# Kernel tuning notes

Hardware: AMD Instinct MI355X
Metric: run time of the kernel (lower is better)

Reference implementation:

```python
import jax, jax.numpy as jnp
import numpy as np

B, T_MEL, F_BINS, C = 32, 1024, 4, 256
S_PHONES = 256
MAX_DUR = 8


def setup_inputs() -> dict:
    key = jax.random.key(0)
    k1, k2 = jax.random.split(key)
    e_src = jax.random.normal(k1, (B, T_MEL, F_BINS, C), dtype=jnp.float32)
    d_src = jax.random.randint(k2, (B, S_PHONES), 0, MAX_DUR, dtype=jnp.int64)
    return {"e_src": e_src, "d_src": d_src}


def reference(e_src, d_src):
    # e_src: [B, T, F, C] prosody features; d_src: [B, S] phone durations (frames).
    # Original: agg[b, i] = mean over dims (0,1) of e_src[b, start_i:start_i+d_i],
    # i.e. mean over (frames_of_phone_i, freq); zeros if the slice is empty.
    Bd, T, Fb, Cd = e_src.shape
    S = d_src.shape[1]
    x = e_src.mean(axis=2)  # [B, T, C] mean over freq (uniform, commutes with frame mean)
    cum = jnp.cumsum(d_src, axis=1)  # [B, S] phone boundary ends
    t = jnp.arange(T)
    # frame -> phone id; frames beyond total duration go to dump segment S
    sid = jax.vmap(lambda c: jnp.searchsorted(c, t, side="right"))(cum)  # [B, T]

    def per_utt(xi, si):
        ssum = jax.ops.segment_sum(xi, si, num_segments=S + 1)[:S]  # [S, C]
        cnt = jax.ops.segment_sum(jnp.ones((T,), xi.dtype), si, num_segments=S + 1)[:S]
        return ssum, cnt

    seg_sum, counts = jax.vmap(per_utt)(x, sid)  # [B,S,C], [B,S]
    mean = seg_sum / jnp.maximum(counts, 1.0)[..., None]
    return jnp.where(counts[..., None] > 0, mean, jnp.zeros((), x.dtype))
```

## Files before the change

### kernel.cpp

```cpp
#include <hip/hip_runtime.h>


#define NB 32
#define NT 1024
#define NF 4
#define NC 256
#define NS 256

__global__ __launch_bounds__(256) void FastSpeech2Pros_83769042141888_kernel(
    const float* __restrict__ e_src,
    const int*   __restrict__ d_src,
    float*       __restrict__ out)
{
    const int s = blockIdx.x;
    const int b = blockIdx.y;
    const int t = threadIdx.x;

    __shared__ int cs[NS];
    cs[t] = d_src[b * NS + t];
    __syncthreads();
    #pragma unroll
    for (int off = 1; off < NS; off <<= 1) {
        int v = (t >= off) ? cs[t - off] : 0;
        __syncthreads();
        cs[t] += v;
        __syncthreads();
    }

    int end   = cs[s];
    int start = (s == 0) ? 0 : cs[s - 1];
    if (start > NT) start = NT;
    if (end   > NT) end   = NT;
    const int cnt = end - start;

    float4 acc = make_float4(0.f, 0.f, 0.f, 0.f);
    const float4* base =
        (const float4*)(e_src + (size_t)b * NT * NF * NC);
    for (int fr = start; fr < end; ++fr) {
        float4 v = base[(size_t)fr * (NF * NC / 4) + t];
        acc.x += v.x; acc.y += v.y; acc.z += v.z; acc.w += v.w;
    }

    __shared__ float4 red[256];
    red[t] = acc;
    __syncthreads();

    if (t < 64) {
        float4 a0 = red[t];
        float4 a1 = red[t + 64];
        float4 a2 = red[t + 128];
        float4 a3 = red[t + 192];
        const float inv = (cnt > 0) ? (1.0f / (4.0f * (float)cnt)) : 0.0f;
        float4 o;
        o.x = (a0.x + a1.x + a2.x + a3.x) * inv;
        o.y = (a0.y + a1.y + a2.y + a3.y) * inv;
        o.z = (a0.z + a1.z + a2.z + a3.z) * inv;
        o.w = (a0.w + a1.w + a2.w + a3.w) * inv;
        ((float4*)(out + ((size_t)b * NS + s) * NC))[t] = o;
    }
}

extern "C" void kernel_launch(void* const* d_in, const int* in_sizes, int n_in,
                              void* d_out, int out_size, void* d_ws, size_t ws_size,
                              hipStream_t stream) {
    const float* e_src = (const float*)d_in[0];
    const int*   d_src = (const int*)d_in[1];
    float*       out   = (float*)d_out;

    dim3 grid(NS, NB);
    FastSpeech2Pros_83769042141888_kernel<<<grid, 256, 0, stream>>>(e_src, d_src, out);
}
```

Before: 190.0 us.

## Assign one wavefront per phone and use shuffle-based prefix scan

```diff
diff --git a/kernel.cpp b/kernel.cpp
--- a/kernel.cpp
+++ b/kernel.cpp
@@ -6,58 +6,58 @@
 #define NF 4
 #define NC 256
 #define NS 256
+#define PPB 4
 
 __global__ __launch_bounds__(256) void FastSpeech2Pros_83769042141888_kernel(
     const float* __restrict__ e_src,
     const int*   __restrict__ d_src,
     float*       __restrict__ out)
 {
-    const int s = blockIdx.x;
-    const int b = blockIdx.y;
-    const int t = threadIdx.x;
+    const int b    = blockIdx.y;
+    const int t    = threadIdx.x;
+    const int lane = t & 63;
+    const int wid  = t >> 6;
 
+    int v = d_src[b * NS + t];
+    #pragma unroll
+    for (int off = 1; off < 64; off <<= 1) {
+        int u = __shfl_up(v, off, 64);
+        if (lane >= off) v += u;
+    }
+    __shared__ int wsum[4];
     __shared__ int cs[NS];
-    cs[t] = d_src[b * NS + t];
+    if (lane == 63) wsum[wid] = v;
     __syncthreads();
+    int woff = 0;
     #pragma unroll
-    for (int off = 1; off < NS; off <<= 1) {
-        int v = (t >= off) ? cs[t - off] : 0;
-        __syncthreads();
-        cs[t] += v;
-        __syncthreads();
-    }
+    for (int w = 0; w < 3; ++w) woff += (w < wid) ? wsum[w] : 0;
+    cs[t] = v + woff;
+    __syncthreads();
 
+    const int s = blockIdx.x * PPB + wid;
     int end   = cs[s];
     int start = (s == 0) ? 0 : cs[s - 1];
     if (start > NT) start = NT;
     if (end   > NT) end   = NT;
     const int cnt = end - start;
 
+    const float4* base4 = (const float4*)(e_src + (size_t)b * NT * NF * NC);
+    const float4* p = base4 + (size_t)start * (NF * NC / 4) + lane;
+
     float4 acc = make_float4(0.f, 0.f, 0.f, 0.f);
-    const float4* base =
-        (const float4*)(e_src + (size_t)b * NT * NF * NC);
-    for (int fr = start; fr < end; ++fr) {
-        float4 v = base[(size_t)fr * (NF * NC / 4) + t];
-        acc.x += v.x; acc.y += v.y; acc.z += v.z; acc.w += v.w;
+    for (int fr = 0; fr < cnt; ++fr) {
+        #pragma unroll
+        for (int f = 0; f < NF; ++f) {
+            float4 x = p[f * 64];
+            acc.x += x.x; acc.y += x.y; acc.z += x.z; acc.w += x.w;
+        }
+        p += NF * NC / 4;
     }
 
-    __shared__ float4 red[256];
-    red[t] = acc;
-    __syncthreads();
-
-    if (t < 64) {
-        float4 a0 = red[t];
-        float4 a1 = red[t + 64];
-        float4 a2 = red[t + 128];
-        float4 a3 = red[t + 192];
-        const float inv = (cnt > 0) ? (1.0f / (4.0f * (float)cnt)) : 0.0f;
-        float4 o;
-        o.x = (a0.x + a1.x + a2.x + a3.x) * inv;
-        o.y = (a0.y + a1.y + a2.y + a3.y) * inv;
-        o.z = (a0.z + a1.z + a2.z + a3.z) * inv;
-        o.w = (a0.w + a1.w + a2.w + a3.w) * inv;
-        ((float4*)(out + ((size_t)b * NS + s) * NC))[t] = o;
-    }
+    const float inv = (cnt > 0) ? (1.0f / (4.0f * (float)cnt)) : 0.0f;
+    float4 o;
+    o.x = acc.x * inv; o.y = acc.y * inv; o.z = acc.z * inv; o.w = acc.w * inv;
+    ((float4*)(out + ((size_t)b * NS + s) * NC))[lane] = o;
 }
 
 extern "C" void kernel_launch(void* const* d_in, const int* in_sizes, int n_in,
@@ -67,6 +67,6 @@
     const int*   d_src = (const int*)d_in[1];
     float*       out   = (float*)d_out;
 
-    dim3 grid(NS, NB);
+    dim3 grid(NS / PPB, NB);
     FastSpeech2Pros_83769042141888_kernel<<<grid, 256, 0, stream>>>(e_src, d_src, out);
 }
```

Result: no change. 190.3 us (+0.2%).
